# Optimization experiments

Measured on AMD Instinct MI355X. Metric: run time of the kernel, lower is better.

The kernel has to match this reference:

```python
import jax, jax.numpy as jnp
import numpy as np

B, D, E, K, H = 16384, 4096, 64, 8, 128


def setup_inputs() -> dict:
    key = jax.random.key(0)
    ks = jax.random.split(key, 6)
    return {
        "r_pooled": jax.random.normal(ks[0], (B, D), jnp.float32),
        "step_frac": jnp.asarray(0.37, jnp.float32),
        "hidden_norm": jax.random.uniform(ks[1], (B,), jnp.float32),
        "confidence": jax.random.uniform(ks[2], (B,), jnp.float32),
        # params stored (in, out); equivalent math to torch Linear
        "W1": jax.random.normal(ks[3], (D + 3, H), jnp.float32) / np.sqrt(D + 3),
        "b1": jnp.zeros((H,), jnp.float32),
        "W2": jax.random.normal(ks[4], (H, E), jnp.float32) / np.sqrt(H),
        "b2": jnp.zeros((E,), jnp.float32),
    }


def reference(r_pooled, step_frac, hidden_norm, confidence, W1, b1, W2, b2):
    b = r_pooled.shape[0]
    step_col = step_frac * jnp.ones((b, 1), r_pooled.dtype)  # torch.full((B,1), step_frac)
    features = jnp.concatenate(
        [r_pooled, step_col, hidden_norm[:, None], confidence[:, None]], axis=-1
    )  # (B, D+3)
    h = jax.nn.silu(features @ W1 + b1)          # (B, 128)
    logits = h @ W2 + b2                         # (B, E)
    topk_vals, topk_idx = jax.lax.top_k(logits, K)
    topk_weights = jax.nn.softmax(topk_vals, axis=-1)
    weights = jnp.zeros_like(logits).at[jnp.arange(b)[:, None], topk_idx].set(topk_weights)
    return weights, logits
```

## Files before the change

kernel.cpp:

```cpp
#include <hip/hip_runtime.h>
#include <math.h>

#define DGL 4096
#define HGL 128
#define EGL 64
#define DELTA 5e-4f

typedef short  short8 __attribute__((ext_vector_type(8)));
typedef float  f32x4  __attribute__((ext_vector_type(4)));

__device__ inline unsigned short bf16_rne(float x) {
    unsigned u = __float_as_uint(x);
    u += 0x7FFFu + ((u >> 16) & 1u);
    return (unsigned short)(u >> 16);
}
__device__ inline void split2(float x, short& hi, short& lo) {
    unsigned u = __float_as_uint(x);
    hi = (short)(u >> 16);
    float hif = __uint_as_float(u & 0xFFFF0000u);
    lo = (short)bf16_rne(x - hif);
}
__device__ inline void split8(const float* f, short8& hi, short8& lo) {
#pragma unroll
    for (int j = 0; j < 8; ++j) { short h, l2; split2(f[j], h, l2); hi[j] = h; lo[j] = l2; }
}

__global__ void pack_w1(const float* __restrict__ W1, unsigned short* __restrict__ wsB1) {
    const int b = blockIdx.x;
    const int kci = b >> 3, nt = b & 7;
    const int l = threadIdx.x, quad = l >> 4, l15 = l & 15;
    short8 vh, vl;
#pragma unroll
    for (int j = 0; j < 8; ++j) {
        const int k = kci * 32 + quad * 8 + j;
        short h, lo; split2(W1[(size_t)k * HGL + nt * 16 + l15], h, lo);
        vh[j] = h; vl[j] = lo;
    }
    *(short8*)(wsB1 + (size_t)kci * 8192 + ((nt * 2 + 0) * 64 + l) * 8) = vh;
    *(short8*)(wsB1 + (size_t)kci * 8192 + ((nt * 2 + 1) * 64 + l) * 8) = vl;
}

__global__ void pack_w2(const float* __restrict__ W2, unsigned short* __restrict__ wsB2,
                        int* __restrict__ gcount) {
    if (blockIdx.x == 0 && threadIdx.x == 0) *gcount = 0;
    const int b = blockIdx.x;
    const int kc2 = b >> 2, nt = b & 3;
    const int l = threadIdx.x, quad = l >> 4, l15 = l & 15;
    short8 vh, vl;
#pragma unroll
    for (int j = 0; j < 8; ++j) {
        const int k = kc2 * 32 + quad * 8 + j;
        short h, lo; split2(W2[k * EGL + nt * 16 + l15], h, lo);
        vh[j] = h; vl[j] = lo;
    }
    *(short8*)(wsB2 + ((kc2 * 4 + nt) * 2 + 0) * 512 + l * 8) = vh;
    *(short8*)(wsB2 + ((kc2 * 4 + nt) * 2 + 1) * 512 + l * 8) = vl;
}

__global__ __launch_bounds__(256, 2) void router_main(
    const float* __restrict__ r_pooled, const float* __restrict__ step_frac,
    const float* __restrict__ hn, const float* __restrict__ cf,
    const float* __restrict__ W1, const float* __restrict__ b1,
    const float* __restrict__ b2v,
    const unsigned short* __restrict__ wsB1, const unsigned short* __restrict__ wsB2,
    int* __restrict__ gcount, int* __restrict__ glist,
    float* __restrict__ out_w, float* __restrict__ out_l)
{
    __shared__ float hsum[32 * 132];
    __shared__ float ls[32 * 65];
    __shared__ float wt[32 * 65];

    const int t = threadIdx.x;
    const int w = t >> 6, l = t & 63;
    const int quad = l >> 4, l15 = l & 15;
    const int row0 = blockIdx.x * 32;

    const float* aB0 = r_pooled + (size_t)(row0 + l15) * DGL + w * 1024 + quad * 8;
    const float* aB1 = aB0 + (size_t)16 * DGL;

    f32x4 acc[2][8];
#pragma unroll
    for (int m = 0; m < 2; ++m)
#pragma unroll
        for (int nt = 0; nt < 8; ++nt) acc[m][nt] = (f32x4){0.f, 0.f, 0.f, 0.f};

    float4 a0[4];
    a0[0] = *(const float4*)(aB0);
    a0[1] = *(const float4*)(aB0 + 4);
    a0[2] = *(const float4*)(aB1);
    a0[3] = *(const float4*)(aB1 + 4);

    for (int kci = 0; kci < 32; ++kci) {
        const int kn = (kci + 1 < 32) ? (kci + 1) : 31;
        float4 a1[4];
        a1[0] = *(const float4*)(aB0 + kn * 32);
        a1[1] = *(const float4*)(aB0 + kn * 32 + 4);
        a1[2] = *(const float4*)(aB1 + kn * 32);
        a1[3] = *(const float4*)(aB1 + kn * 32 + 4);

        const unsigned short* bp = wsB1 + (size_t)(w * 32 + kci) * 8192 + l * 8;
        short8 b[16];
#pragma unroll
        for (int nt = 0; nt < 8; ++nt) {
            b[2 * nt]     = *(const short8*)(bp + (2 * nt) * 512);
            b[2 * nt + 1] = *(const short8*)(bp + (2 * nt + 1) * 512);
        }

        short8 ahi[2], alo[2];
#pragma unroll
        for (int m = 0; m < 2; ++m) {
            float fa[8];
#pragma unroll
            for (int j = 0; j < 4; ++j) { fa[j] = a0[2 * m][j]; fa[j + 4] = a0[2 * m + 1][j]; }
            split8(fa, ahi[m], alo[m]);
        }
#pragma unroll
        for (int m = 0; m < 2; ++m)
#pragma unroll
            for (int nt = 0; nt < 8; ++nt) {
                acc[m][nt] = __builtin_amdgcn_mfma_f32_16x16x32_bf16(ahi[m], b[2 * nt],     acc[m][nt], 0, 0, 0);
                acc[m][nt] = __builtin_amdgcn_mfma_f32_16x16x32_bf16(ahi[m], b[2 * nt + 1], acc[m][nt], 0, 0, 0);
                acc[m][nt] = __builtin_amdgcn_mfma_f32_16x16x32_bf16(alo[m], b[2 * nt],     acc[m][nt], 0, 0, 0);
            }
#pragma unroll
        for (int i = 0; i < 4; ++i) a0[i] = a1[i];
    }

    if (w == 0) {
#pragma unroll
        for (int m = 0; m < 2; ++m)
#pragma unroll
            for (int nt = 0; nt < 8; ++nt)
#pragma unroll
                for (int r = 0; r < 4; ++r)
                    hsum[(m * 16 + quad * 4 + r) * 132 + nt * 16 + l15] = acc[m][nt][r];
    }
    __syncthreads();
#pragma unroll
    for (int wv = 1; wv < 4; ++wv) {
        if (w == wv) {
#pragma unroll
            for (int m = 0; m < 2; ++m)
#pragma unroll
                for (int nt = 0; nt < 8; ++nt)
#pragma unroll
                    for (int r = 0; r < 4; ++r)
                        hsum[(m * 16 + quad * 4 + r) * 132 + nt * 16 + l15] += acc[m][nt][r];
        }
        __syncthreads();
    }

    {
        const float sf = step_frac[0];
#pragma unroll
        for (int j = 0; j < 16; ++j) {
            const int idx = j * 256 + t;
            const int r = idx >> 7, c = idx & 127;
            float x = hsum[r * 132 + c];
            x += sf * W1[(size_t)4096 * HGL + c]
               + hn[row0 + r] * W1[(size_t)4097 * HGL + c]
               + cf[row0 + r] * W1[(size_t)4098 * HGL + c] + b1[c];
            hsum[r * 132 + c] = x / (1.0f + expf(-x));
        }
    }
    __syncthreads();

    const int mt2 = w >> 1, nh2 = w & 1;
    f32x4 acc2[2];
    acc2[0] = (f32x4){0.f, 0.f, 0.f, 0.f};
    acc2[1] = (f32x4){0.f, 0.f, 0.f, 0.f};
#pragma unroll
    for (int kc2 = 0; kc2 < 4; ++kc2) {
        const float4 va = *(const float4*)&hsum[(mt2 * 16 + l15) * 132 + kc2 * 32 + quad * 8];
        const float4 vb = *(const float4*)&hsum[(mt2 * 16 + l15) * 132 + kc2 * 32 + quad * 8 + 4];
        float fa[8];
#pragma unroll
        for (int j = 0; j < 4; ++j) { fa[j] = ((const float*)&va)[j]; fa[j + 4] = ((const float*)&vb)[j]; }
        short8 h2, lo2;
        split8(fa, h2, lo2);
#pragma unroll
        for (int ntp = 0; ntp < 2; ++ntp) {
            const int nt = nh2 * 2 + ntp;
            const short8 bh = *(const short8*)(wsB2 + ((kc2 * 4 + nt) * 2 + 0) * 512 + l * 8);
            const short8 bl = *(const short8*)(wsB2 + ((kc2 * 4 + nt) * 2 + 1) * 512 + l * 8);
            acc2[ntp] = __builtin_amdgcn_mfma_f32_16x16x32_bf16(h2,  bh, acc2[ntp], 0, 0, 0);
            acc2[ntp] = __builtin_amdgcn_mfma_f32_16x16x32_bf16(h2,  bl, acc2[ntp], 0, 0, 0);
            acc2[ntp] = __builtin_amdgcn_mfma_f32_16x16x32_bf16(lo2, bh, acc2[ntp], 0, 0, 0);
        }
    }

#pragma unroll
    for (int ntp = 0; ntp < 2; ++ntp) {
        const int c = (nh2 * 2 + ntp) * 16 + l15;
        const float bv = b2v[c];
#pragma unroll
        for (int r = 0; r < 4; ++r) {
            const int lr = mt2 * 16 + quad * 4 + r;
            const float v = acc2[ntp][r] + bv;
            out_l[(size_t)(row0 + lr) * EGL + c] = v;
            ls[lr * 65 + c] = v;
        }
    }
    for (int i = t; i < 32 * 65; i += 256) wt[i] = 0.0f;
    __syncthreads();

    if (t < 32) {
        float vals[9]; int idxs[9];
#pragma unroll
        for (int i = 0; i < 9; ++i) { vals[i] = -INFINITY; idxs[i] = 0; }
        for (int e = 0; e < EGL; ++e) {
            const float v = ls[t * 65 + e];
            if (v > vals[8]) {
                int p = 8;
                while (p > 0 && v > vals[p - 1]) { vals[p] = vals[p - 1]; idxs[p] = idxs[p - 1]; --p; }
                vals[p] = v; idxs[p] = e;
            }
        }
        const float mx = vals[0];
        float wgt[8], ssum = 0.0f;
#pragma unroll
        for (int i = 0; i < 8; ++i) { wgt[i] = expf(vals[i] - mx); ssum += wgt[i]; }
        const float inv = 1.0f / ssum;
#pragma unroll
        for (int i = 0; i < 8; ++i) wt[t * 65 + idxs[i]] = wgt[i] * inv;
        if (vals[7] - vals[8] < DELTA) {
            int p = atomicAdd(gcount, 1);
            if (p < 16384) glist[p] = row0 + t;
        }
    }
    __syncthreads();

    for (int i = t; i < 32 * EGL; i += 256) {
        const int m = i >> 6, c = i & 63;
        out_w[(size_t)(row0 + m) * EGL + c] = wt[m * 65 + c];
    }
}

__global__ __launch_bounds__(512, 1) void refine_rows(
    const float* __restrict__ r_pooled, const float* __restrict__ step_frac,
    const float* __restrict__ hn, const float* __restrict__ cf,
    const float* __restrict__ W1, const float* __restrict__ b1,
    const float* __restrict__ W2, const float* __restrict__ b2,
    const int* __restrict__ gcount, const int* __restrict__ glist,
    float* __restrict__ out_w)
{
    __shared__ __align__(16) float als[DGL];
    __shared__ float part[4][128];
    __shared__ float hred[128];
    __shared__ float lb[64];
    __shared__ float wb[64];

    const int t = threadIdx.x;
    const int cnt = *gcount;
    const int c = t & 127, sl = t >> 7;

    for (int i = blockIdx.x; i < cnt; i += gridDim.x) {
        const int row = glist[i];
        __syncthreads();
        for (int j = t; j < DGL / 4; j += 512)
            *(float4*)&als[j * 4] = *(const float4*)&r_pooled[(size_t)row * DGL + j * 4];
        __syncthreads();

        float pr = 0.0f;
        const float* ap = als + sl * 1024;
        const float* wp = W1 + (size_t)(sl * 1024) * HGL + c;
#pragma unroll 8
        for (int k = 0; k < 1024; ++k) pr = fmaf(ap[k], wp[(size_t)k * HGL], pr);
        part[sl][c] = pr;
        __syncthreads();

        if (t < 128) {
            const float sf = step_frac[0];
            float x = part[0][t] + part[1][t] + part[2][t] + part[3][t];
            x += sf * W1[(size_t)4096 * HGL + t] + hn[row] * W1[(size_t)4097 * HGL + t]
               + cf[row] * W1[(size_t)4098 * HGL + t] + b1[t];
            hred[t] = x / (1.0f + expf(-x));
        }
        __syncthreads();
        if (t < 64) {
            float a = b2[t];
            for (int k = 0; k < HGL; ++k) a = fmaf(hred[k], W2[k * EGL + t], a);
            lb[t] = a; wb[t] = 0.0f;
        }
        __syncthreads();
        if (t == 0) {
            float vals[8]; int idxs[8];
#pragma unroll
            for (int q = 0; q < 8; ++q) { vals[q] = -INFINITY; idxs[q] = 0; }
            for (int e = 0; e < EGL; ++e) {
                const float v = lb[e];
                if (v > vals[7]) {
                    int p = 7;
                    while (p > 0 && v > vals[p - 1]) { vals[p] = vals[p - 1]; idxs[p] = idxs[p - 1]; --p; }
                    vals[p] = v; idxs[p] = e;
                }
            }
            const float mx = vals[0];
            float wgt[8], ssum = 0.0f;
#pragma unroll
            for (int q = 0; q < 8; ++q) { wgt[q] = expf(vals[q] - mx); ssum += wgt[q]; }
            const float inv = 1.0f / ssum;
#pragma unroll
            for (int q = 0; q < 8; ++q) wb[idxs[q]] = wgt[q] * inv;
        }
        __syncthreads();
        if (t < 64) out_w[(size_t)row * EGL + t] = wb[t];
    }
}

extern "C" void kernel_launch(void* const* d_in, const int* in_sizes, int n_in,
                              void* d_out, int out_size, void* d_ws, size_t ws_size,
                              hipStream_t stream) {
    const float* r_pooled    = (const float*)d_in[0];
    const float* step_frac   = (const float*)d_in[1];
    const float* hidden_norm = (const float*)d_in[2];
    const float* confidence  = (const float*)d_in[3];
    const float* W1          = (const float*)d_in[4];
    const float* b1          = (const float*)d_in[5];
    const float* W2          = (const float*)d_in[6];
    const float* b2          = (const float*)d_in[7];

    const int B = in_sizes[2];
    float* out_w = (float*)d_out;
    float* out_l = out_w + (size_t)B * EGL;

    unsigned short* wsB1 = (unsigned short*)d_ws;
    unsigned short* wsB2 = (unsigned short*)((char*)d_ws + 2097152);
    int* gcount = (int*)((char*)d_ws + 2129920);
    int* glist  = (int*)((char*)d_ws + 2129984);

    hipLaunchKernelGGL(pack_w1, dim3(1024), dim3(64), 0, stream, W1, wsB1);
    hipLaunchKernelGGL(pack_w2, dim3(16), dim3(64), 0, stream, W2, wsB2, gcount);
    hipLaunchKernelGGL(router_main, dim3(B / 32), dim3(256), 0, stream,
                       r_pooled, step_frac, hidden_norm, confidence,
                       W1, b1, b2, wsB1, wsB2, gcount, glist, out_w, out_l);
    hipLaunchKernelGGL(refine_rows, dim3(256), dim3(512), 0, stream,
                       r_pooled, step_frac, hidden_norm, confidence,
                       W1, b1, W2, b2, gcount, glist, out_w);
}
```

Baseline: 561.7 us.

## Split router_main K-reduction across eight waves with dual shared-memory partial sums

Doubles the router_main block to 512 threads so eight waves each cover 512 of the 4096 input columns, halving the per-wave K loop. Partial accumulators are reduced into two shared buffers (hsum and hsum2), which are then summed in the SiLU epilogue. The second GEMM is re-split so each of the eight waves owns one 16x16 output tile. The aim is more latency hiding and memory-level parallelism for the bandwidth-bound first GEMM. The cost is extra shared memory and a longer serialized reduction, and the launch bounds of (512,4) press hard on the register budget for the 16-wide accumulator array.

```diff
diff --git a/kernel.cpp b/kernel.cpp
--- a/kernel.cpp
+++ b/kernel.cpp
@@ -57,7 +57,7 @@
     *(short8*)(wsB2 + ((kc2 * 4 + nt) * 2 + 1) * 512 + l * 8) = vl;
 }
 
-__global__ __launch_bounds__(256, 2) void router_main(
+__global__ __launch_bounds__(512, 4) void router_main(
     const float* __restrict__ r_pooled, const float* __restrict__ step_frac,
     const float* __restrict__ hn, const float* __restrict__ cf,
     const float* __restrict__ W1, const float* __restrict__ b1,
@@ -67,6 +67,7 @@
     float* __restrict__ out_w, float* __restrict__ out_l)
 {
     __shared__ float hsum[32 * 132];
+    __shared__ float hsum2[32 * 132];
     __shared__ float ls[32 * 65];
     __shared__ float wt[32 * 65];
 
@@ -75,7 +76,7 @@
     const int quad = l >> 4, l15 = l & 15;
     const int row0 = blockIdx.x * 32;
 
-    const float* aB0 = r_pooled + (size_t)(row0 + l15) * DGL + w * 1024 + quad * 8;
+    const float* aB0 = r_pooled + (size_t)(row0 + l15) * DGL + w * 512 + quad * 8;
     const float* aB1 = aB0 + (size_t)16 * DGL;
 
     f32x4 acc[2][8];
@@ -90,15 +91,15 @@
     a0[2] = *(const float4*)(aB1);
     a0[3] = *(const float4*)(aB1 + 4);
 
-    for (int kci = 0; kci < 32; ++kci) {
-        const int kn = (kci + 1 < 32) ? (kci + 1) : 31;
+    for (int kci = 0; kci < 16; ++kci) {
+        const int kn = (kci + 1 < 16) ? (kci + 1) : 15;
         float4 a1[4];
         a1[0] = *(const float4*)(aB0 + kn * 32);
         a1[1] = *(const float4*)(aB0 + kn * 32 + 4);
         a1[2] = *(const float4*)(aB1 + kn * 32);
         a1[3] = *(const float4*)(aB1 + kn * 32 + 4);
 
-        const unsigned short* bp = wsB1 + (size_t)(w * 32 + kci) * 8192 + l * 8;
+        const unsigned short* bp = wsB1 + (size_t)(w * 16 + kci) * 8192 + l * 8;
         short8 b[16];
 #pragma unroll
         for (int nt = 0; nt < 8; ++nt) {
@@ -135,6 +136,15 @@
                 for (int r = 0; r < 4; ++r)
                     hsum[(m * 16 + quad * 4 + r) * 132 + nt * 16 + l15] = acc[m][nt][r];
     }
+    if (w == 4) {
+#pragma unroll
+        for (int m = 0; m < 2; ++m)
+#pragma unroll
+            for (int nt = 0; nt < 8; ++nt)
+#pragma unroll
+                for (int r = 0; r < 4; ++r)
+                    hsum2[(m * 16 + quad * 4 + r) * 132 + nt * 16 + l15] = acc[m][nt][r];
+    }
     __syncthreads();
 #pragma unroll
     for (int wv = 1; wv < 4; ++wv) {
@@ -147,16 +157,25 @@
                     for (int r = 0; r < 4; ++r)
                         hsum[(m * 16 + quad * 4 + r) * 132 + nt * 16 + l15] += acc[m][nt][r];
         }
+        if (w == wv + 4) {
+#pragma unroll
+            for (int m = 0; m < 2; ++m)
+#pragma unroll
+                for (int nt = 0; nt < 8; ++nt)
+#pragma unroll
+                    for (int r = 0; r < 4; ++r)
+                        hsum2[(m * 16 + quad * 4 + r) * 132 + nt * 16 + l15] += acc[m][nt][r];
+        }
         __syncthreads();
     }
 
     {
         const float sf = step_frac[0];
 #pragma unroll
-        for (int j = 0; j < 16; ++j) {
-            const int idx = j * 256 + t;
+        for (int j = 0; j < 8; ++j) {
+            const int idx = j * 512 + t;
             const int r = idx >> 7, c = idx & 127;
-            float x = hsum[r * 132 + c];
+            float x = hsum[r * 132 + c] + hsum2[r * 132 + c];
             x += sf * W1[(size_t)4096 * HGL + c]
                + hn[row0 + r] * W1[(size_t)4097 * HGL + c]
                + cf[row0 + r] * W1[(size_t)4098 * HGL + c] + b1[c];
@@ -165,10 +184,8 @@
     }
     __syncthreads();
 
-    const int mt2 = w >> 1, nh2 = w & 1;
-    f32x4 acc2[2];
-    acc2[0] = (f32x4){0.f, 0.f, 0.f, 0.f};
-    acc2[1] = (f32x4){0.f, 0.f, 0.f, 0.f};
+    const int mt2 = w >> 2, nt2 = w & 3;
+    f32x4 acc2 = (f32x4){0.f, 0.f, 0.f, 0.f};
 #pragma unroll
     for (int kc2 = 0; kc2 < 4; ++kc2) {
         const float4 va = *(const float4*)&hsum[(mt2 * 16 + l15) * 132 + kc2 * 32 + quad * 8];
@@ -178,30 +195,25 @@
         for (int j = 0; j < 4; ++j) { fa[j] = ((const float*)&va)[j]; fa[j + 4] = ((const float*)&vb)[j]; }
         short8 h2, lo2;
         split8(fa, h2, lo2);
-#pragma unroll
-        for (int ntp = 0; ntp < 2; ++ntp) {
-            const int nt = nh2 * 2 + ntp;
-            const short8 bh = *(const short8*)(wsB2 + ((kc2 * 4 + nt) * 2 + 0) * 512 + l * 8);
-            const short8 bl = *(const short8*)(wsB2 + ((kc2 * 4 + nt) * 2 + 1) * 512 + l * 8);
-            acc2[ntp] = __builtin_amdgcn_mfma_f32_16x16x32_bf16(h2,  bh, acc2[ntp], 0, 0, 0);
-            acc2[ntp] = __builtin_amdgcn_mfma_f32_16x16x32_bf16(h2,  bl, acc2[ntp], 0, 0, 0);
-            acc2[ntp] = __builtin_amdgcn_mfma_f32_16x16x32_bf16(lo2, bh, acc2[ntp], 0, 0, 0);
-        }
-    }
-
-#pragma unroll
-    for (int ntp = 0; ntp < 2; ++ntp) {
-        const int c = (nh2 * 2 + ntp) * 16 + l15;
+        const short8 bh = *(const short8*)(wsB2 + ((kc2 * 4 + nt2) * 2 + 0) * 512 + l * 8);
+        const short8 bl = *(const short8*)(wsB2 + ((kc2 * 4 + nt2) * 2 + 1) * 512 + l * 8);
+        acc2 = __builtin_amdgcn_mfma_f32_16x16x32_bf16(h2,  bh, acc2, 0, 0, 0);
+        acc2 = __builtin_amdgcn_mfma_f32_16x16x32_bf16(h2,  bl, acc2, 0, 0, 0);
+        acc2 = __builtin_amdgcn_mfma_f32_16x16x32_bf16(lo2, bh, acc2, 0, 0, 0);
+    }
+
+    {
+        const int c = nt2 * 16 + l15;
         const float bv = b2v[c];
 #pragma unroll
         for (int r = 0; r < 4; ++r) {
             const int lr = mt2 * 16 + quad * 4 + r;
-            const float v = acc2[ntp][r] + bv;
+            const float v = acc2[r] + bv;
             out_l[(size_t)(row0 + lr) * EGL + c] = v;
             ls[lr * 65 + c] = v;
         }
     }
-    for (int i = t; i < 32 * 65; i += 256) wt[i] = 0.0f;
+    for (int i = t; i < 32 * 65; i += 512) wt[i] = 0.0f;
     __syncthreads();
 
     if (t < 32) {
@@ -230,7 +242,7 @@
     }
     __syncthreads();
 
-    for (int i = t; i < 32 * EGL; i += 256) {
+    for (int i = t; i < 32 * EGL; i += 512) {
         const int m = i >> 6, c = i & 63;
         out_w[(size_t)(row0 + m) * EGL + c] = wt[m * 65 + c];
     }
@@ -331,7 +343,7 @@
 
     hipLaunchKernelGGL(pack_w1, dim3(1024), dim3(64), 0, stream, W1, wsB1);
     hipLaunchKernelGGL(pack_w2, dim3(16), dim3(64), 0, stream, W2, wsB2, gcount);
-    hipLaunchKernelGGL(router_main, dim3(B / 32), dim3(256), 0, stream,
+    hipLaunchKernelGGL(router_main, dim3(B / 32), dim3(512), 0, stream,
                        r_pooled, step_frac, hidden_norm, confidence,
                        W1, b1, b2, wsB1, wsB2, gcount, glist, out_w, out_l);
     hipLaunchKernelGGL(refine_rows, dim3(256), dim3(512), 0, stream,
```

After: 742.5 us. 32.2% more time.

## Stage packed W1 tiles in LDS via async loads shared across 64-row blocks

Applied to the files above, without the earlier changes.

Each router block now processes 64 rows with 512 threads. The packed bf16 hi/lo W1 chunks are brought into a double-buffered LDS region with global_load_lds, so two waves covering different row halves share one copy instead of each reloading it from global memory. The r_pooled prefetch is folded into the same pipeline, and B fragments are software-prefetched from LDS inside the MFMA loop. This trades occupancy (one 512-thread block per CU, 128KB LDS) for less W1 traffic. Correctness relies on the async LDS loads completing before the barrier, which the code does not explicitly wait for.

```diff
diff --git a/kernel.cpp b/kernel.cpp
--- a/kernel.cpp
+++ b/kernel.cpp
@@ -23,6 +23,11 @@
 __device__ inline void split8(const float* f, short8& hi, short8& lo) {
 #pragma unroll
     for (int j = 0; j < 8; ++j) { short h, l2; split2(f[j], h, l2); hi[j] = h; lo[j] = l2; }
+}
+
+__device__ inline void gload_lds16(const void* g, void* l) {
+    __builtin_amdgcn_global_load_lds((const __attribute__((address_space(1))) void*)g,
+                                     (__attribute__((address_space(3))) void*)l, 16, 0, 0);
 }
 
 __global__ void pack_w1(const float* __restrict__ W1, unsigned short* __restrict__ wsB1) {
@@ -57,7 +62,7 @@
     *(short8*)(wsB2 + ((kc2 * 4 + nt) * 2 + 1) * 512 + l * 8) = vl;
 }
 
-__global__ __launch_bounds__(256, 2) void router_main(
+__global__ __launch_bounds__(512, 1) void router_main(
     const float* __restrict__ r_pooled, const float* __restrict__ step_frac,
     const float* __restrict__ hn, const float* __restrict__ cf,
     const float* __restrict__ W1, const float* __restrict__ b1,
@@ -66,16 +71,15 @@
     int* __restrict__ gcount, int* __restrict__ glist,
     float* __restrict__ out_w, float* __restrict__ out_l)
 {
-    __shared__ float hsum[32 * 132];
-    __shared__ float ls[32 * 65];
-    __shared__ float wt[32 * 65];
+    __shared__ __align__(16) char smem[131072];
 
     const int t = threadIdx.x;
     const int w = t >> 6, l = t & 63;
     const int quad = l >> 4, l15 = l & 15;
-    const int row0 = blockIdx.x * 32;
-
-    const float* aB0 = r_pooled + (size_t)(row0 + l15) * DGL + w * 1024 + quad * 8;
+    const int row0 = blockIdx.x * 64;
+    const int kq = w & 3, mh = w >> 2;
+
+    const float* aB0 = r_pooled + (size_t)(row0 + mh * 32 + l15) * DGL + kq * 1024 + quad * 8;
     const float* aB1 = aB0 + (size_t)16 * DGL;
 
     f32x4 acc[2][8];
@@ -84,28 +88,23 @@
 #pragma unroll
         for (int nt = 0; nt < 8; ++nt) acc[m][nt] = (f32x4){0.f, 0.f, 0.f, 0.f};
 
+    const char* wsB1b = (const char*)wsB1;
+
+    {
+        const char* gs = wsB1b + (size_t)(kq * 32 + 0) * 16384 + mh * 8192 + (size_t)l * 16;
+        char* lp = smem + kq * 16384 + mh * 8192;
+#pragma unroll
+        for (int c = 0; c < 8; ++c) gload_lds16(gs + c * 1024, lp + c * 1024);
+    }
+    asm volatile("" ::: "memory");
     float4 a0[4];
     a0[0] = *(const float4*)(aB0);
     a0[1] = *(const float4*)(aB0 + 4);
     a0[2] = *(const float4*)(aB1);
     a0[3] = *(const float4*)(aB1 + 4);
 
+    int s = 0;
     for (int kci = 0; kci < 32; ++kci) {
-        const int kn = (kci + 1 < 32) ? (kci + 1) : 31;
-        float4 a1[4];
-        a1[0] = *(const float4*)(aB0 + kn * 32);
-        a1[1] = *(const float4*)(aB0 + kn * 32 + 4);
-        a1[2] = *(const float4*)(aB1 + kn * 32);
-        a1[3] = *(const float4*)(aB1 + kn * 32 + 4);
-
-        const unsigned short* bp = wsB1 + (size_t)(w * 32 + kci) * 8192 + l * 8;
-        short8 b[16];
-#pragma unroll
-        for (int nt = 0; nt < 8; ++nt) {
-            b[2 * nt]     = *(const short8*)(bp + (2 * nt) * 512);
-            b[2 * nt + 1] = *(const short8*)(bp + (2 * nt + 1) * 512);
-        }
-
         short8 ahi[2], alo[2];
 #pragma unroll
         for (int m = 0; m < 2; ++m) {
@@ -114,38 +113,68 @@
             for (int j = 0; j < 4; ++j) { fa[j] = a0[2 * m][j]; fa[j + 4] = a0[2 * m + 1][j]; }
             split8(fa, ahi[m], alo[m]);
         }
+
+        __builtin_amdgcn_sched_barrier(0);
+        __builtin_amdgcn_s_barrier();
+
+        if (kci + 1 < 32) {
+            const char* gs = wsB1b + (size_t)(kq * 32 + kci + 1) * 16384 + mh * 8192 + (size_t)l * 16;
+            char* lp = smem + (s ^ 1) * 65536 + kq * 16384 + mh * 8192;
+#pragma unroll
+            for (int c = 0; c < 8; ++c) gload_lds16(gs + c * 1024, lp + c * 1024);
+            asm volatile("" ::: "memory");
+            a0[0] = *(const float4*)(aB0 + (kci + 1) * 32);
+            a0[1] = *(const float4*)(aB0 + (kci + 1) * 32 + 4);
+            a0[2] = *(const float4*)(aB1 + (kci + 1) * 32);
+            a0[3] = *(const float4*)(aB1 + (kci + 1) * 32 + 4);
+        }
+
+        const char* bp = smem + s * 65536 + kq * 16384 + (size_t)l * 16;
+        short8 bh = *(const short8*)(bp + 0 * 1024);
+        short8 bl = *(const short8*)(bp + 1 * 1024);
+#pragma unroll
+        for (int nt = 0; nt < 8; ++nt) {
+            short8 bhn, bln;
+            if (nt < 7) {
+                bhn = *(const short8*)(bp + (2 * nt + 2) * 1024);
+                bln = *(const short8*)(bp + (2 * nt + 3) * 1024);
+            }
+            acc[0][nt] = __builtin_amdgcn_mfma_f32_16x16x32_bf16(ahi[0], bh, acc[0][nt], 0, 0, 0);
+            acc[0][nt] = __builtin_amdgcn_mfma_f32_16x16x32_bf16(ahi[0], bl, acc[0][nt], 0, 0, 0);
+            acc[0][nt] = __builtin_amdgcn_mfma_f32_16x16x32_bf16(alo[0], bh, acc[0][nt], 0, 0, 0);
+            acc[1][nt] = __builtin_amdgcn_mfma_f32_16x16x32_bf16(ahi[1], bh, acc[1][nt], 0, 0, 0);
+            acc[1][nt] = __builtin_amdgcn_mfma_f32_16x16x32_bf16(ahi[1], bl, acc[1][nt], 0, 0, 0);
+            acc[1][nt] = __builtin_amdgcn_mfma_f32_16x16x32_bf16(alo[1], bh, acc[1][nt], 0, 0, 0);
+            bh = bhn; bl = bln;
+        }
+        s ^= 1;
+    }
+    __syncthreads();
+
+    float* hsum = (float*)smem;
+    float* ls   = (float*)(smem + 33792);
+    float* wt   = (float*)(smem + 50432);
+
+    if (kq == 0) {
 #pragma unroll
         for (int m = 0; m < 2; ++m)
 #pragma unroll
-            for (int nt = 0; nt < 8; ++nt) {
-                acc[m][nt] = __builtin_amdgcn_mfma_f32_16x16x32_bf16(ahi[m], b[2 * nt],     acc[m][nt], 0, 0, 0);
-                acc[m][nt] = __builtin_amdgcn_mfma_f32_16x16x32_bf16(ahi[m], b[2 * nt + 1], acc[m][nt], 0, 0, 0);
-                acc[m][nt] = __builtin_amdgcn_mfma_f32_16x16x32_bf16(alo[m], b[2 * nt],     acc[m][nt], 0, 0, 0);
-            }
-#pragma unroll
-        for (int i = 0; i < 4; ++i) a0[i] = a1[i];
-    }
-
-    if (w == 0) {
-#pragma unroll
-        for (int m = 0; m < 2; ++m)
-#pragma unroll
             for (int nt = 0; nt < 8; ++nt)
 #pragma unroll
                 for (int r = 0; r < 4; ++r)
-                    hsum[(m * 16 + quad * 4 + r) * 132 + nt * 16 + l15] = acc[m][nt][r];
+                    hsum[(mh * 32 + m * 16 + quad * 4 + r) * 132 + nt * 16 + l15] = acc[m][nt][r];
     }
     __syncthreads();
 #pragma unroll
     for (int wv = 1; wv < 4; ++wv) {
-        if (w == wv) {
+        if (kq == wv) {
 #pragma unroll
             for (int m = 0; m < 2; ++m)
 #pragma unroll
                 for (int nt = 0; nt < 8; ++nt)
 #pragma unroll
                     for (int r = 0; r < 4; ++r)
-                        hsum[(m * 16 + quad * 4 + r) * 132 + nt * 16 + l15] += acc[m][nt][r];
+                        hsum[(mh * 32 + m * 16 + quad * 4 + r) * 132 + nt * 16 + l15] += acc[m][nt][r];
         }
         __syncthreads();
     }
@@ -154,7 +183,7 @@
         const float sf = step_frac[0];
 #pragma unroll
         for (int j = 0; j < 16; ++j) {
-            const int idx = j * 256 + t;
+            const int idx = j * 512 + t;
             const int r = idx >> 7, c = idx & 127;
             float x = hsum[r * 132 + c];
             x += sf * W1[(size_t)4096 * HGL + c]
@@ -201,10 +230,10 @@
             ls[lr * 65 + c] = v;
         }
     }
-    for (int i = t; i < 32 * 65; i += 256) wt[i] = 0.0f;
-    __syncthreads();
-
-    if (t < 32) {
+    for (int i = t; i < 64 * 65; i += 512) wt[i] = 0.0f;
+    __syncthreads();
+
+    if (t < 64) {
         float vals[9]; int idxs[9];
 #pragma unroll
         for (int i = 0; i < 9; ++i) { vals[i] = -INFINITY; idxs[i] = 0; }
@@ -230,7 +259,7 @@
     }
     __syncthreads();
 
-    for (int i = t; i < 32 * EGL; i += 256) {
+    for (int i = t; i < 64 * EGL; i += 512) {
         const int m = i >> 6, c = i & 63;
         out_w[(size_t)(row0 + m) * EGL + c] = wt[m * 65 + c];
     }
@@ -331,7 +360,7 @@
 
     hipLaunchKernelGGL(pack_w1, dim3(1024), dim3(64), 0, stream, W1, wsB1);
     hipLaunchKernelGGL(pack_w2, dim3(16), dim3(64), 0, stream, W2, wsB2, gcount);
-    hipLaunchKernelGGL(router_main, dim3(B / 32), dim3(256), 0, stream,
+    hipLaunchKernelGGL(router_main, dim3(B / 64), dim3(512), 0, stream,
                        r_pooled, step_frac, hidden_norm, confidence,
                        W1, b1, b2, wsB1, wsB2, gcount, glist, out_w, out_l);
     hipLaunchKernelGGL(refine_rows, dim3(256), dim3(512), 0, stream,
```

After: 545.7 us. 1.03x faster.
